# Optimization experiments

Measured on AMD Instinct MI355X. Metric: run time of the kernel, lower is better.

The kernel has to match this reference:

```python
import jax, jax.numpy as jnp
import numpy as np

IN_, OUT_, HID, B = 1024, 1024, 4, 8192

def setup_inputs() -> dict:
    key = jax.random.key(0)
    k_x, k_w1, k_b1, k_w2, k_b2 = jax.random.split(key, 5)
    x = jax.random.normal(k_x, (B, IN_), dtype=jnp.float32)
    # Stacked params for out_ tiny MLPs: Linear(in,4) -> LeakyReLU(0.1) -> Linear(4,1)
    s1 = 1.0 / np.sqrt(IN_)
    s2 = 1.0 / np.sqrt(HID)
    W1 = jax.random.uniform(k_w1, (OUT_, IN_, HID), dtype=jnp.float32, minval=-s1, maxval=s1)
    b1 = jax.random.uniform(k_b1, (OUT_, HID), dtype=jnp.float32, minval=-s1, maxval=s1)
    W2 = jax.random.uniform(k_w2, (OUT_, HID), dtype=jnp.float32, minval=-s2, maxval=s2)
    b2 = jax.random.uniform(k_b2, (OUT_,), dtype=jnp.float32, minval=-s2, maxval=s2)
    return {"x": x, "W1": W1, "b1": b1, "W2": W2, "b2": b2}

def reference(x, W1, b1, W2, b2):
    # h[b,o,h] = x[b,:] @ W1[o] + b1[o]  (shared input across all out_ MLPs)
    h = jnp.einsum('bi,oih->boh', x, W1) + b1
    h = jnp.where(h >= 0, h, 0.1 * h)  # LeakyReLU(0.1)
    # out[b,o] = h[b,o,:] @ W2[o] + b2[o]; equals torch.cat of per-MLP scalars
    out = jnp.einsum('boh,oh->bo', h, W2) + b2
    return out
```

## Files before the change

### kernel.cpp

```cpp
#include <hip/hip_runtime.h>
#include <hip/hip_bf16.h>

#define IN_DIM  1024
#define OUT_DIM 1024
#define HID     4
#define BATCH   8192
#define NCOL    (OUT_DIM * HID)

typedef __bf16 bf16x8 __attribute__((ext_vector_type(8)));
typedef float  f32x4  __attribute__((ext_vector_type(4)));
typedef float  f32x16 __attribute__((ext_vector_type(16)));

__device__ __forceinline__ unsigned short f2bf(float f) {
  union { float f; unsigned int u; } v; v.f = f;
  unsigned int u = v.u;
  u += 0x7FFFu + ((u >> 16) & 1u);
  return (unsigned short)(u >> 16);
}

__global__ __launch_bounds__(256) void cvt_x_kernel(const float4* __restrict__ in,
                                                    ushort4* __restrict__ out) {
  int i = blockIdx.x * 256 + threadIdx.x;
  float4 v = in[i];
  ushort4 o;
  o.x = f2bf(v.x); o.y = f2bf(v.y); o.z = f2bf(v.z); o.w = f2bf(v.w);
  out[i] = o;
}

__global__ __launch_bounds__(256) void cvt_w1t_kernel(const float* __restrict__ W1,
                                                      ushort4* __restrict__ out) {
  int b = blockIdx.x;
  int g = ((b & 7) * ((int)gridDim.x >> 3) + (b >> 3)) * 256 + threadIdx.x;
  int i4 = g & 255;
  int oh = g >> 8;
  int h = oh & 3, o = oh >> 2;
  const float* src = W1 + (size_t)o * 4096 + h;
  ushort4 r;
  r.x = f2bf(src[(i4 * 4 + 0) * 4]);
  r.y = f2bf(src[(i4 * 4 + 1) * 4]);
  r.z = f2bf(src[(i4 * 4 + 2) * 4]);
  r.w = f2bf(src[(i4 * 4 + 3) * 4]);
  out[(size_t)oh * 256 + i4] = r;
}

__device__ __forceinline__ void gload16(const void* g, void* l) {
  __builtin_amdgcn_global_load_lds(
      (const __attribute__((address_space(1))) unsigned int*)g,
      (__attribute__((address_space(3))) unsigned int*)l, 16, 0, 0);
}

__global__ __launch_bounds__(256, 2) void mlp_gemm_kernel(
    const unsigned short* __restrict__ A,
    const unsigned short* __restrict__ Bm,
    const f32x4* __restrict__ b1v,
    const f32x4* __restrict__ w2v,
    const float* __restrict__ b2,
    float* __restrict__ out) {
  __shared__ __align__(16) unsigned short lds[36864];

  const int bid = blockIdx.x;
  const int xcd = bid & 7, loc = bid >> 3;
  const int bm = loc >> 3;
  const int bn = xcd * 8 + (loc & 7);
  const int tileM = bm * 256, tileN = bn * 128;

  const int t = threadIdx.x;
  const int lane = t & 63, wid = t >> 6;
  const int wm = wid >> 1, wn = wid & 1;
  const int l31 = lane & 31, hi = lane >> 5;

  const int sr = t >> 2;
  const int sc = (((t & 3) ^ ((sr >> 1) & 3)) << 3);
  const unsigned short* Abase = A  + (size_t)(tileM + sr) * IN_DIM + sc;
  const unsigned short* Bbase = Bm + (size_t)(tileN + sr) * IN_DIM + sc;

  auto stage = [&](int kt, int p) {
    const int kb = kt * 32;
    unsigned short* lA = lds + p * 12288 + t * 8;
#pragma unroll
    for (int i = 0; i < 4; ++i)
      gload16(Abase + (size_t)i * 64 * IN_DIM + kb, lA + i * 2048);
#pragma unroll
    for (int i = 0; i < 2; ++i)
      gload16(Bbase + (size_t)i * 64 * IN_DIM + kb, lA + 8192 + i * 2048);
  };

  f32x16 acc[4][2];
#pragma unroll
  for (int m = 0; m < 4; ++m)
#pragma unroll
    for (int n = 0; n < 2; ++n)
#pragma unroll
      for (int r = 0; r < 16; ++r) acc[m][n][r] = 0.f;

  const int swz = (l31 >> 1) & 3;
  const int p0 = (hi ^ swz) * 8;
  const int p1 = ((2 + hi) ^ swz) * 8;
  const int arow = (wm * 128 + l31) * 32;
  const int brow = 8192 + (wn * 64 + l31) * 32;

  stage(0, 0);
  stage(1, 1);
  asm volatile("s_waitcnt vmcnt(6)" ::: "memory");
  __builtin_amdgcn_s_barrier();
  __builtin_amdgcn_sched_barrier(0);

  auto ktile = [&](int kt, int pr, int ps, int mode) {
    if (mode == 0) stage(kt + 2, ps);
    const unsigned short* bufp = lds + pr * 12288;
    bf16x8 a0[4], b0[2], a1[4], b1_[2];
    a0[0] = *(const bf16x8*)(bufp + arow + 0 * 1024 + p0);
    b0[0] = *(const bf16x8*)(bufp + brow + 0 * 1024 + p0);
    b0[1] = *(const bf16x8*)(bufp + brow + 1 * 1024 + p0);
    a0[1] = *(const bf16x8*)(bufp + arow + 1 * 1024 + p0);
    a0[2] = *(const bf16x8*)(bufp + arow + 2 * 1024 + p0);
    a0[3] = *(const bf16x8*)(bufp + arow + 3 * 1024 + p0);
    a1[0] = *(const bf16x8*)(bufp + arow + 0 * 1024 + p1);
    b1_[0] = *(const bf16x8*)(bufp + brow + 0 * 1024 + p1);
    b1_[1] = *(const bf16x8*)(bufp + brow + 1 * 1024 + p1);
    a1[1] = *(const bf16x8*)(bufp + arow + 1 * 1024 + p1);
    a1[2] = *(const bf16x8*)(bufp + arow + 2 * 1024 + p1);
    a1[3] = *(const bf16x8*)(bufp + arow + 3 * 1024 + p1);
#pragma unroll
    for (int mf = 0; mf < 4; ++mf)
#pragma unroll
      for (int nf = 0; nf < 2; ++nf)
        acc[mf][nf] = __builtin_amdgcn_mfma_f32_32x32x16_bf16(a0[mf], b0[nf], acc[mf][nf], 0, 0, 0);
#pragma unroll
    for (int mf = 0; mf < 4; ++mf)
#pragma unroll
      for (int nf = 0; nf < 2; ++nf)
        acc[mf][nf] = __builtin_amdgcn_mfma_f32_32x32x16_bf16(a1[mf], b1_[nf], acc[mf][nf], 0, 0, 0);
    if (mode == 0)      asm volatile("s_waitcnt vmcnt(6)" ::: "memory");
    else if (mode == 1) asm volatile("s_waitcnt vmcnt(0)" ::: "memory");
    if (mode < 2) {
      __builtin_amdgcn_s_barrier();
      __builtin_amdgcn_sched_barrier(0);
    }
  };

  for (int g = 0; g < 30; g += 3) {
    ktile(g,     0, 2, 0);
    ktile(g + 1, 1, 0, 0);
    ktile(g + 2, 2, 1, 0);
  }
  ktile(30, 0, 0, 1);
  ktile(31, 1, 0, 2);
  __syncthreads();

  float* LE = (float*)lds;
  const int obase = tileM >> 2;
#pragma unroll
  for (int mf = 0; mf < 4; ++mf) {
#pragma unroll
    for (int g = 0; g < 4; ++g) {
      int o_loc = wm * 32 + mf * 8 + 2 * g + hi;
      f32x4 b1q = b1v[obase + o_loc];
      f32x4 w2q = w2v[obase + o_loc];
#pragma unroll
      for (int nf = 0; nf < 2; ++nf) {
        int bat = wn * 64 + nf * 32 + l31;
        float v = 0.f;
#pragma unroll
        for (int h = 0; h < 4; ++h) {
          float hj = acc[mf][nf][4 * g + h] + b1q[h];
          hj = (hj >= 0.f) ? hj : 0.1f * hj;
          v += hj * w2q[h];
        }
        LE[bat * 65 + o_loc] = v;
      }
    }
  }
  __syncthreads();

  const int col = t & 63, rowb = t >> 6;
  const float b2s = b2[obase + col];
  float* outB = out + (size_t)tileN * OUT_DIM + obase;
#pragma unroll
  for (int i = 0; i < 32; ++i) {
    int row = rowb + i * 4;
    outB[(size_t)row * OUT_DIM + col] = LE[row * 65 + col] + b2s;
  }
}

__global__ __launch_bounds__(256) void fallback_kernel(
    const float* __restrict__ x, const float* __restrict__ W1,
    const float* __restrict__ b1, const float* __restrict__ W2,
    const float* __restrict__ b2, float* __restrict__ out) {
  int idx = blockIdx.x * 256 + threadIdx.x;
  if (idx >= BATCH * OUT_DIM) return;
  int bb = idx >> 10, o = idx & 1023;
  const float4* w1p = (const float4*)(W1 + (size_t)o * 4096);
  const float*  xp  = x + (size_t)bb * 1024;
  float4 acc = *(const float4*)(b1 + o * 4);
  for (int i = 0; i < 1024; ++i) {
    float xv = xp[i];
    float4 w = w1p[i];
    acc.x += xv * w.x; acc.y += xv * w.y; acc.z += xv * w.z; acc.w += xv * w.w;
  }
  float4 w2 = *(const float4*)(W2 + o * 4);
  float r = b2[o];
  r += ((acc.x >= 0.f) ? acc.x : 0.1f * acc.x) * w2.x;
  r += ((acc.y >= 0.f) ? acc.y : 0.1f * acc.y) * w2.y;
  r += ((acc.z >= 0.f) ? acc.z : 0.1f * acc.z) * w2.z;
  r += ((acc.w >= 0.f) ? acc.w : 0.1f * acc.w) * w2.w;
  out[(size_t)bb * OUT_DIM + o] = r;
}

extern "C" void kernel_launch(void* const* d_in, const int* in_sizes, int n_in,
                              void* d_out, int out_size, void* d_ws, size_t ws_size,
                              hipStream_t stream) {
  const float* x  = (const float*)d_in[0];
  const float* W1 = (const float*)d_in[1];
  const float* b1 = (const float*)d_in[2];
  const float* W2 = (const float*)d_in[3];
  const float* b2 = (const float*)d_in[4];
  float* out = (float*)d_out;

  size_t need = (size_t)BATCH * IN_DIM * 2 + (size_t)NCOL * IN_DIM * 2;
  if (ws_size >= need) {
    unsigned short* xbf = (unsigned short*)d_ws;
    unsigned short* w1t = xbf + (size_t)BATCH * IN_DIM;
    cvt_x_kernel<<<(BATCH * IN_DIM / 4) / 256, 256, 0, stream>>>((const float4*)x, (ushort4*)xbf);
    cvt_w1t_kernel<<<(NCOL * IN_DIM / 4) / 256, 256, 0, stream>>>(W1, (ushort4*)w1t);
    mlp_gemm_kernel<<<(NCOL / 256) * (BATCH / 128), 256, 0, stream>>>(
        w1t, xbf, (const f32x4*)b1, (const f32x4*)W2, b2, out);
  } else {
    fallback_kernel<<<(BATCH * OUT_DIM + 255) / 256, 256, 0, stream>>>(x, W1, b1, W2, b2, out);
  }
}
```

Before: 95.36 us.

## Enlarge GEMM tile to 256x256 with BK=64 double buffering

Grows the per-block output tile from 256x128 to 256x256 and the K step from 32 to 64. Pipelining changes from a three-stage ring with partial vmcnt waits to a two-buffer scheme with an 8-way XOR swizzle and full waits each iteration. Each wave now holds 16 accumulator fragments, which is meant to raise MFMA work per LDS and global byte and halve the number of blocks. In exchange, occupancy drops to one block per CU because LDS use and register pressure rise. The epilogue is widened to write 256 batch rows per block.

Result: faster. 92.81 us (-2.7%).

```diff
diff --git a/kernel.cpp b/kernel.cpp
--- a/kernel.cpp
+++ b/kernel.cpp
@@ -49,103 +49,86 @@
       (__attribute__((address_space(3))) unsigned int*)l, 16, 0, 0);
 }
 
-__global__ __launch_bounds__(256, 2) void mlp_gemm_kernel(
+__global__ __launch_bounds__(256, 1) void mlp_gemm_kernel(
     const unsigned short* __restrict__ A,
     const unsigned short* __restrict__ Bm,
     const f32x4* __restrict__ b1v,
     const f32x4* __restrict__ w2v,
     const float* __restrict__ b2,
     float* __restrict__ out) {
-  __shared__ __align__(16) unsigned short lds[36864];
+  __shared__ __align__(16) unsigned short lds[65536];
 
   const int bid = blockIdx.x;
   const int xcd = bid & 7, loc = bid >> 3;
-  const int bm = loc >> 3;
-  const int bn = xcd * 8 + (loc & 7);
-  const int tileM = bm * 256, tileN = bn * 128;
+  const int bn = xcd * 4 + (loc & 3);
+  const int bm = loc >> 2;
+  const int tileM = bm * 256, tileN = bn * 256;
 
   const int t = threadIdx.x;
   const int lane = t & 63, wid = t >> 6;
   const int wm = wid >> 1, wn = wid & 1;
   const int l31 = lane & 31, hi = lane >> 5;
 
-  const int sr = t >> 2;
-  const int sc = (((t & 3) ^ ((sr >> 1) & 3)) << 3);
-  const unsigned short* Abase = A  + (size_t)(tileM + sr) * IN_DIM + sc;
-  const unsigned short* Bbase = Bm + (size_t)(tileN + sr) * IN_DIM + sc;
+  const int sr8 = t >> 3, slt = t & 7;
+  const int scol = ((slt ^ (sr8 & 7)) << 3);
+  const unsigned short* Asrc = A  + (size_t)(tileM + sr8) * IN_DIM + scol;
+  const unsigned short* Bsrc = Bm + (size_t)(tileN + sr8) * IN_DIM + scol;
 
   auto stage = [&](int kt, int p) {
-    const int kb = kt * 32;
-    unsigned short* lA = lds + p * 12288 + t * 8;
-#pragma unroll
-    for (int i = 0; i < 4; ++i)
-      gload16(Abase + (size_t)i * 64 * IN_DIM + kb, lA + i * 2048);
-#pragma unroll
-    for (int i = 0; i < 2; ++i)
-      gload16(Bbase + (size_t)i * 64 * IN_DIM + kb, lA + 8192 + i * 2048);
-  };
-
-  f32x16 acc[4][2];
-#pragma unroll
-  for (int m = 0; m < 4; ++m)
-#pragma unroll
-    for (int n = 0; n < 2; ++n)
-#pragma unroll
-      for (int r = 0; r < 16; ++r) acc[m][n][r] = 0.f;
-
-  const int swz = (l31 >> 1) & 3;
-  const int p0 = (hi ^ swz) * 8;
-  const int p1 = ((2 + hi) ^ swz) * 8;
-  const int arow = (wm * 128 + l31) * 32;
-  const int brow = 8192 + (wn * 64 + l31) * 32;
-
-  stage(0, 0);
-  stage(1, 1);
-  asm volatile("s_waitcnt vmcnt(6)" ::: "memory");
-  __builtin_amdgcn_s_barrier();
-  __builtin_amdgcn_sched_barrier(0);
-
-  auto ktile = [&](int kt, int pr, int ps, int mode) {
-    if (mode == 0) stage(kt + 2, ps);
-    const unsigned short* bufp = lds + pr * 12288;
-    bf16x8 a0[4], b0[2], a1[4], b1_[2];
-    a0[0] = *(const bf16x8*)(bufp + arow + 0 * 1024 + p0);
-    b0[0] = *(const bf16x8*)(bufp + brow + 0 * 1024 + p0);
-    b0[1] = *(const bf16x8*)(bufp + brow + 1 * 1024 + p0);
-    a0[1] = *(const bf16x8*)(bufp + arow + 1 * 1024 + p0);
-    a0[2] = *(const bf16x8*)(bufp + arow + 2 * 1024 + p0);
-    a0[3] = *(const bf16x8*)(bufp + arow + 3 * 1024 + p0);
-    a1[0] = *(const bf16x8*)(bufp + arow + 0 * 1024 + p1);
-    b1_[0] = *(const bf16x8*)(bufp + brow + 0 * 1024 + p1);
-    b1_[1] = *(const bf16x8*)(bufp + brow + 1 * 1024 + p1);
-    a1[1] = *(const bf16x8*)(bufp + arow + 1 * 1024 + p1);
-    a1[2] = *(const bf16x8*)(bufp + arow + 2 * 1024 + p1);
-    a1[3] = *(const bf16x8*)(bufp + arow + 3 * 1024 + p1);
-#pragma unroll
-    for (int mf = 0; mf < 4; ++mf)
-#pragma unroll
-      for (int nf = 0; nf < 2; ++nf)
-        acc[mf][nf] = __builtin_amdgcn_mfma_f32_32x32x16_bf16(a0[mf], b0[nf], acc[mf][nf], 0, 0, 0);
-#pragma unroll
-    for (int mf = 0; mf < 4; ++mf)
-#pragma unroll
-      for (int nf = 0; nf < 2; ++nf)
-        acc[mf][nf] = __builtin_amdgcn_mfma_f32_32x32x16_bf16(a1[mf], b1_[nf], acc[mf][nf], 0, 0, 0);
-    if (mode == 0)      asm volatile("s_waitcnt vmcnt(6)" ::: "memory");
-    else if (mode == 1) asm volatile("s_waitcnt vmcnt(0)" ::: "memory");
-    if (mode < 2) {
-      __builtin_amdgcn_s_barrier();
-      __builtin_amdgcn_sched_barrier(0);
+    const int kb = kt * 64;
+    unsigned short* lA = lds + p * 32768 + t * 8;
+    unsigned short* lB = lA + 16384;
+#pragma unroll
+    for (int i = 0; i < 8; ++i) {
+      gload16(Asrc + (size_t)(32 * i) * IN_DIM + kb, lA + i * 2048);
+      gload16(Bsrc + (size_t)(32 * i) * IN_DIM + kb, lB + i * 2048);
     }
   };
 
-  for (int g = 0; g < 30; g += 3) {
-    ktile(g,     0, 2, 0);
-    ktile(g + 1, 1, 0, 0);
-    ktile(g + 2, 2, 1, 0);
-  }
-  ktile(30, 0, 0, 1);
-  ktile(31, 1, 0, 2);
+  f32x16 acc[4][4];
+#pragma unroll
+  for (int m = 0; m < 4; ++m)
+#pragma unroll
+    for (int n = 0; n < 4; ++n)
+#pragma unroll
+      for (int r = 0; r < 16; ++r) acc[m][n][r] = 0.f;
+
+  const int rsw = l31 & 7;
+
+  stage(0, 0);
+  asm volatile("s_waitcnt vmcnt(0)" ::: "memory");
+  __builtin_amdgcn_s_barrier();
+
+  for (int kt = 0; kt < 16; ++kt) {
+    const int cur = kt & 1;
+    if (kt < 15) stage(kt + 1, cur ^ 1);
+
+    const unsigned short* bufp = lds + cur * 32768;
+    const unsigned short* aR = bufp + (wm * 128 + l31) * 64;
+    const unsigned short* bR = bufp + 16384 + (wn * 128 + l31) * 64;
+
+#pragma unroll
+    for (int ks = 0; ks < 4; ++ks) {
+      const int pk = ((2 * ks + hi) ^ rsw) << 3;
+      bf16x8 a[4], b[4];
+      a[0] = *(const bf16x8*)(aR + 0 * 2048 + pk);
+      b[0] = *(const bf16x8*)(bR + 0 * 2048 + pk);
+      b[1] = *(const bf16x8*)(bR + 1 * 2048 + pk);
+      b[2] = *(const bf16x8*)(bR + 2 * 2048 + pk);
+      b[3] = *(const bf16x8*)(bR + 3 * 2048 + pk);
+      a[1] = *(const bf16x8*)(aR + 1 * 2048 + pk);
+      a[2] = *(const bf16x8*)(aR + 2 * 2048 + pk);
+      a[3] = *(const bf16x8*)(aR + 3 * 2048 + pk);
+#pragma unroll
+      for (int mf = 0; mf < 4; ++mf)
+#pragma unroll
+        for (int nf = 0; nf < 4; ++nf)
+          acc[mf][nf] = __builtin_amdgcn_mfma_f32_32x32x16_bf16(a[mf], b[nf], acc[mf][nf], 0, 0, 0);
+    }
+
+    if (kt < 15) asm volatile("s_waitcnt vmcnt(0)" ::: "memory");
+    __builtin_amdgcn_s_barrier();
+  }
   __syncthreads();
 
   float* LE = (float*)lds;
@@ -158,8 +141,8 @@
       f32x4 b1q = b1v[obase + o_loc];
       f32x4 w2q = w2v[obase + o_loc];
 #pragma unroll
-      for (int nf = 0; nf < 2; ++nf) {
-        int bat = wn * 64 + nf * 32 + l31;
+      for (int nf = 0; nf < 4; ++nf) {
+        int bat = wn * 128 + nf * 32 + l31;
         float v = 0.f;
 #pragma unroll
         for (int h = 0; h < 4; ++h) {
@@ -177,7 +160,7 @@
   const float b2s = b2[obase + col];
   float* outB = out + (size_t)tileN * OUT_DIM + obase;
 #pragma unroll
-  for (int i = 0; i < 32; ++i) {
+  for (int i = 0; i < 64; ++i) {
     int row = rowb + i * 4;
     outB[(size_t)row * OUT_DIM + col] = LE[row * 65 + col] + b2s;
   }
@@ -223,7 +206,7 @@
     unsigned short* w1t = xbf + (size_t)BATCH * IN_DIM;
     cvt_x_kernel<<<(BATCH * IN_DIM / 4) / 256, 256, 0, stream>>>((const float4*)x, (ushort4*)xbf);
     cvt_w1t_kernel<<<(NCOL * IN_DIM / 4) / 256, 256, 0, stream>>>(W1, (ushort4*)w1t);
-    mlp_gemm_kernel<<<(NCOL / 256) * (BATCH / 128), 256, 0, stream>>>(
+    mlp_gemm_kernel<<<(NCOL / 256) * (BATCH / 256), 256, 0, stream>>>(
         w1t, xbf, (const f32x4*)b1, (const f32x4*)W2, b2, out);
   } else {
     fallback_kernel<<<(BATCH * OUT_DIM + 255) / 256, 256, 0, stream>>>(x, W1, b1, W2, b2, out);
```
